# Optimization experiments

Measured on AMD Instinct MI355X. Metric: run time of the kernel, lower is better.

## Reference

```python
import jax, jax.numpy as jnp
import numpy as np

QMAX = 7.0  # 4-bit symmetric: levels in [-8, 7]

def quant4(w):
    # per-tensor symmetric 4-bit fake-quant with straight-through estimator
    s = jnp.max(jnp.abs(w)) / QMAX
    q = jnp.clip(jnp.round(w / s), -8.0, 7.0) * s
    return w + jax.lax.stop_gradient(q - w)

def setup_inputs() -> dict:
    key = jax.random.key(0)
    ks = jax.random.split(key, 7)
    B = 2048
    x = jax.random.normal(ks[0], (B, 1, 31, 16, 31), dtype=jnp.float32)
    # conv: out_ch=1, in_ch=1, kernel (5,3,5)
    w_conv = jax.random.normal(ks[1], (1, 1, 5, 3, 5), dtype=jnp.float32) * 0.1
    b_conv = jax.random.normal(ks[2], (1,), dtype=jnp.float32) * 0.1
    w_fc1 = jax.random.normal(ks[3], (128, 343), dtype=jnp.float32) * 0.05
    b_fc1 = jax.random.normal(ks[4], (128,), dtype=jnp.float32) * 0.05
    w_fc2 = jax.random.normal(ks[5], (4, 128), dtype=jnp.float32) * 0.05
    b_fc2 = jax.random.normal(ks[6], (4,), dtype=jnp.float32) * 0.05
    return {"x": x, "w_conv": w_conv, "b_conv": b_conv,
            "w_fc1": w_fc1, "b_fc1": b_fc1, "w_fc2": w_fc2, "b_fc2": b_fc2}

def reference(x, w_conv, b_conv, w_fc1, b_fc1, w_fc2, b_fc2):
    # QuantConv3d: 4-bit quantized weights, stride (2,1,2), no padding
    c1 = jax.lax.conv_general_dilated(
        x, quant4(w_conv), window_strides=(2, 1, 2), padding='VALID',
        dimension_numbers=('NCDHW', 'OIDHW', 'NCDHW'))
    c1 = c1 + b_conv.reshape(1, -1, 1, 1, 1)          # [B,1,14,14,14]
    # MaxPool3d(2)
    p1 = jax.lax.reduce_window(c1, -jnp.inf, jax.lax.max,
                               (1, 1, 2, 2, 2), (1, 1, 2, 2, 2), 'VALID')  # [B,1,7,7,7]
    f = p1.reshape(p1.shape[0], -1)                   # [B,343]
    a1 = jax.nn.relu(f @ quant4(w_fc1).T + b_fc1)     # [B,128]
    s2 = a1 @ quant4(w_fc2).T + b_fc2                 # [B,4]
    return jax.nn.softmax(s2, axis=1)
```

## Files before the change

kernel.cpp:

```cpp
#include <hip/hip_runtime.h>
#include <hip/hip_bf16.h>

#define WS_WCONV   128
#define WS_W1T     256
#define WS_W2      44160

__device__ __forceinline__ float q4(float w, float s) {
  if (s <= 0.f) return 0.f;
  float r = rintf(w / s);
  r = fminf(fmaxf(r, -8.f), 7.f);
  return r * s;
}

__global__ __launch_bounds__(256) void quant_all(
    const float* __restrict__ wconv, const float* __restrict__ w1,
    const float* __restrict__ w2, float* __restrict__ ws) {
  __shared__ float red[256];
  int b = blockIdx.x, t = threadIdx.x;
  if (b < 88) {
    const float4* w4 = (const float4*)w1;
    float m = 0.f;
    for (int i = t; i < 10976; i += 256) {
      float4 v = w4[i];
      m = fmaxf(m, fmaxf(fmaxf(fabsf(v.x), fabsf(v.y)),
                         fmaxf(fabsf(v.z), fabsf(v.w))));
    }
    red[t] = m;
    __syncthreads();
    for (int s = 128; s > 0; s >>= 1) {
      if (t < s) red[t] = fmaxf(red[t], red[t + s]);
      __syncthreads();
    }
    float s = red[0] * (1.0f / 7.0f);
    #pragma unroll
    for (int k = 0; k < 2; ++k) {
      int idx = b * 512 + k * 256 + t;
      if (idx < 43904) {
        float q = q4(w1[idx], s);
        int o = idx / 343;
        int j = idx - o * 343;
        ws[WS_W1T + j * 128 + o] = q;
      }
    }
  } else {
    float mc = (t < 75) ? fabsf(wconv[t]) : 0.f;
    float m2 = 0.f;
    for (int i = t; i < 512; i += 256) m2 = fmaxf(m2, fabsf(w2[i]));
    red[t] = mc;
    __syncthreads();
    for (int s = 128; s > 0; s >>= 1) {
      if (t < s) red[t] = fmaxf(red[t], red[t + s]);
      __syncthreads();
    }
    float sc = red[0] * (1.0f / 7.0f);
    __syncthreads();
    red[t] = m2;
    __syncthreads();
    for (int s = 128; s > 0; s >>= 1) {
      if (t < s) red[t] = fmaxf(red[t], red[t + s]);
      __syncthreads();
    }
    float s2 = red[0] * (1.0f / 7.0f);
    if (t < 75) ws[WS_WCONV + t] = q4(wconv[t], sc);
    #pragma unroll
    for (int k = 0; k < 2; ++k) {
      int idx = k * 256 + t;
      ws[WS_W2 + idx] = q4(w2[idx], s2);
    }
  }
}

__device__ __forceinline__ void conv_phase(
    const float* __restrict__ xs, const float* __restrict__ wq,
    int t, int npf, int pd_off, float bc, float* __restrict__ feat) {
  if (t >= npf) return;
  int pdl = t / 49;
  int rr  = t - pdl * 49;
  int ph  = rr / 7;
  int pw  = rr - ph * 7;
  float c[2][2][2];
  #pragma unroll
  for (int i = 0; i < 8; ++i) ((float*)c)[i] = 0.f;
  int base0 = pdl * 1984 + ph * 62 + pw * 4;
  #pragma unroll
  for (int dd = 0; dd < 7; ++dd) {
    int rbase = base0 + dd * 496;
    #pragma unroll
    for (int hh = 0; hh < 4; ++hh) {
      float row[7];
      #pragma unroll
      for (int wi = 0; wi < 7; ++wi) row[wi] = xs[rbase + hh * 31 + wi];
      #pragma unroll
      for (int odp = 0; odp < 2; ++odp) {
        int kd = dd - 2 * odp;
        if (kd < 0 || kd > 4) continue;
        #pragma unroll
        for (int ohp = 0; ohp < 2; ++ohp) {
          int kh = hh - ohp;
          if (kh < 0 || kh > 2) continue;
          #pragma unroll
          for (int owp = 0; owp < 2; ++owp) {
            float a = c[odp][ohp][owp];
            #pragma unroll
            for (int kw = 0; kw < 5; ++kw)
              a = fmaf(row[2 * owp + kw], wq[kd * 15 + kh * 5 + kw], a);
            c[odp][ohp][owp] = a;
          }
        }
      }
    }
  }
  float m = ((float*)c)[0];
  #pragma unroll
  for (int i = 1; i < 8; ++i) m = fmaxf(m, ((float*)c)[i]);
  feat[(pdl + pd_off) * 49 + rr] = m + bc;
}

__global__ __launch_bounds__(256, 4) void fused_net(
    const float* __restrict__ x, const float* __restrict__ bconv,
    const float* __restrict__ ws, const float* __restrict__ bfc1,
    const float* __restrict__ bfc2, float* __restrict__ out) {
  __shared__ float xs[9424];
  __shared__ float feat[344];
  __shared__ float fc1p[128];
  __shared__ float a1[128];
  __shared__ float s2[4];
  int t = threadIdx.x;
  int b = blockIdx.x;
  const float* wq = ws + WS_WCONV;
  float bc = bconv[0];

  {
    const float4* src = (const float4*)(x + (size_t)b * 15376);
    float4* dst = (float4*)xs;
    for (int i = t; i < 2356; i += 256) dst[i] = src[i];
    if (t == 0) feat[343] = 0.f;
  }
  __syncthreads();
  conv_phase(xs, wq, t, 196, 0, bc, feat);
  __syncthreads();
  {
    const float4* src = (const float4*)(x + (size_t)b * 15376 + 16 * 496);
    float4* dst = (float4*)xs;
    for (int i = t; i < 1860; i += 256) dst[i] = src[i];
  }
  __syncthreads();
  conv_phase(xs, wq, t, 147, 4, bc, feat);
  __syncthreads();

  int g = t >> 7, o = t & 127;
  {
    const float* w1T = ws + WS_W1T;
    int j0 = g ? 172 : 0;
    const float4* f4 = (const float4*)&feat[j0];
    const float* wp = w1T + j0 * 128 + o;
    float p0 = 0.f, p1 = 0.f, p2 = 0.f, p3 = 0.f;
    for (int q = 0; q < 43; ++q) {
      float4 ff = f4[q];
      p0 = fmaf(ff.x, wp[0],   p0);
      p1 = fmaf(ff.y, wp[128], p1);
      p2 = fmaf(ff.z, wp[256], p2);
      p3 = fmaf(ff.w, wp[384], p3);
      wp += 512;
    }
    float acc = (p0 + p1) + (p2 + p3);
    if (g) fc1p[o] = acc;
    __syncthreads();
    if (!g) a1[o] = fmaxf(acc + fc1p[o] + bfc1[o], 0.f);
  }
  __syncthreads();

  if (t < 64) {
    int cls = t & 3, kk = t >> 2;
    const float* w2 = ws + WS_W2 + cls * 128 + kk * 8;
    const float* av = a1 + kk * 8;
    float p = 0.f;
    #pragma unroll
    for (int i = 0; i < 8; ++i) p = fmaf(av[i], w2[i], p);
    p += __shfl_down(p, 32);
    p += __shfl_down(p, 16);
    p += __shfl_down(p, 8);
    p += __shfl_down(p, 4);
    if (t < 4) s2[t] = p + bfc2[t];
  }
  __syncthreads();
  if (t < 4) {
    float v0 = s2[0], v1 = s2[1], v2 = s2[2], v3 = s2[3];
    float m = fmaxf(fmaxf(v0, v1), fmaxf(v2, v3));
    float e0 = expf(v0 - m), e1 = expf(v1 - m);
    float e2 = expf(v2 - m), e3 = expf(v3 - m);
    float inv = 1.f / (e0 + e1 + e2 + e3);
    float mine = (t == 0) ? e0 : (t == 1) ? e1 : (t == 2) ? e2 : e3;
    out[b * 4 + t] = mine * inv;
  }
}

extern "C" void kernel_launch(void* const* d_in, const int* in_sizes, int n_in,
                              void* d_out, int out_size, void* d_ws, size_t ws_size,
                              hipStream_t stream) {
  const float* x     = (const float*)d_in[0];
  const float* wconv = (const float*)d_in[1];
  const float* bconv = (const float*)d_in[2];
  const float* wfc1  = (const float*)d_in[3];
  const float* bfc1  = (const float*)d_in[4];
  const float* wfc2  = (const float*)d_in[5];
  const float* bfc2  = (const float*)d_in[6];
  float* out = (float*)d_out;
  float* ws  = (float*)d_ws;

  quant_all<<<89, 256, 0, stream>>>(wconv, wfc1, wfc2, ws);
  fused_net<<<2048, 256, 0, stream>>>(x, bconv, ws, bfc1, bfc2, out);
}
```

Baseline: 227.6 us.

## Swizzle shared input rows to padded layout and prefetch second half during conv

Stores the input tile in shared memory as rows padded to 32 floats with an XOR swizzle on 4-float groups, so each conv thread reads its 7-wide window with two float4 loads instead of seven scalar loads, with fewer bank conflicts. The second half of the input is loaded into registers before the first conv phase, so the global load overlaps with compute. Small scratch arrays now alias the input buffer. The price is more address arithmetic in the scatter, higher register pressure from the prefetch registers, and a larger shared allocation that may lower occupancy.

```diff
diff --git a/kernel.cpp b/kernel.cpp
--- a/kernel.cpp
+++ b/kernel.cpp
@@ -1,5 +1,4 @@
 #include <hip/hip_runtime.h>
-#include <hip/hip_bf16.h>
 
 #define WS_WCONV   128
 #define WS_W1T     256
@@ -70,6 +69,23 @@
   }
 }
 
+__device__ __forceinline__ void scat1(float* xs, int r, int c, float v) {
+  xs[(r << 5) + (((c >> 2) ^ (r & 7)) << 2) + (c & 3)] = v;
+}
+
+__device__ __forceinline__ void scatter4(float* xs, float4 v, int i) {
+  int e0 = i << 2;
+  int r  = (int)(((unsigned)e0 * 67651u) >> 21);
+  int c  = e0 - r * 31;
+  int c1 = c + 1, r1 = r; if (c1 >= 31) { c1 -= 31; ++r1; }
+  int c2 = c + 2, r2 = r; if (c2 >= 31) { c2 -= 31; ++r2; }
+  int c3 = c + 3, r3 = r; if (c3 >= 31) { c3 -= 31; ++r3; }
+  scat1(xs, r,  c,  v.x);
+  scat1(xs, r1, c1, v.y);
+  scat1(xs, r2, c2, v.z);
+  scat1(xs, r3, c3, v.w);
+}
+
 __device__ __forceinline__ void conv_phase(
     const float* __restrict__ xs, const float* __restrict__ wq,
     int t, int npf, int pd_off, float bc, float* __restrict__ feat) {
@@ -81,15 +97,19 @@
   float c[2][2][2];
   #pragma unroll
   for (int i = 0; i < 8; ++i) ((float*)c)[i] = 0.f;
-  int base0 = pdl * 1984 + ph * 62 + pw * 4;
+  int h0 = 2 * ph;
+  int dbase = pdl * 2048;
   #pragma unroll
   for (int dd = 0; dd < 7; ++dd) {
-    int rbase = base0 + dd * 496;
+    int rb = dbase + dd * 512;
     #pragma unroll
     for (int hh = 0; hh < 4; ++hh) {
-      float row[7];
-      #pragma unroll
-      for (int wi = 0; wi < 7; ++wi) row[wi] = xs[rbase + hh * 31 + wi];
+      int h = h0 + hh;
+      int rowb = rb + (h << 5);
+      int sw = h & 7;
+      float4 A = *(const float4*)(xs + rowb + ((pw ^ sw) << 2));
+      float4 B = *(const float4*)(xs + rowb + (((pw + 1) ^ sw) << 2));
+      float row[7] = {A.x, A.y, A.z, A.w, B.x, B.y, B.z};
       #pragma unroll
       for (int odp = 0; odp < 2; ++odp) {
         int kd = dd - 2 * odp;
@@ -120,11 +140,11 @@
     const float* __restrict__ x, const float* __restrict__ bconv,
     const float* __restrict__ ws, const float* __restrict__ bfc1,
     const float* __restrict__ bfc2, float* __restrict__ out) {
-  __shared__ float xs[9424];
-  __shared__ float feat[344];
-  __shared__ float fc1p[128];
-  __shared__ float a1[128];
-  __shared__ float s2[4];
+  __shared__ alignas(16) float xs[9728];
+  __shared__ alignas(16) float feat[344];
+  float* fc1p = xs;
+  float* a1   = xs + 128;
+  float* s2   = xs + 256;
   int t = threadIdx.x;
   int b = blockIdx.x;
   const float* wq = ws + WS_WCONV;
@@ -132,19 +152,55 @@
 
   {
     const float4* src = (const float4*)(x + (size_t)b * 15376);
-    float4* dst = (float4*)xs;
-    for (int i = t; i < 2356; i += 256) dst[i] = src[i];
+    float4 v0 = src[t];
+    float4 v1 = src[t + 256];
+    float4 v2 = src[t + 512];
+    float4 v3 = src[t + 768];
+    float4 v4 = src[t + 1024];
+    float4 v5 = src[t + 1280];
+    float4 v6 = src[t + 1536];
+    float4 v7 = src[t + 1792];
+    float4 v8 = src[t + 2048];
+    bool has9 = (t + 2304) < 2356;
+    float4 v9 = has9 ? src[t + 2304] : make_float4(0.f, 0.f, 0.f, 0.f);
+    scatter4(xs, v0, t);
+    scatter4(xs, v1, t + 256);
+    scatter4(xs, v2, t + 512);
+    scatter4(xs, v3, t + 768);
+    scatter4(xs, v4, t + 1024);
+    scatter4(xs, v5, t + 1280);
+    scatter4(xs, v6, t + 1536);
+    scatter4(xs, v7, t + 1792);
+    scatter4(xs, v8, t + 2048);
+    if (has9) scatter4(xs, v9, t + 2304);
     if (t == 0) feat[343] = 0.f;
   }
   __syncthreads();
+
+  const float4* src2 = (const float4*)(x + (size_t)b * 15376 + 7936);
+  float4 p0 = src2[t];
+  float4 p1 = src2[t + 256];
+  float4 p2 = src2[t + 512];
+  float4 p3 = src2[t + 768];
+  float4 p4 = src2[t + 1024];
+  float4 p5 = src2[t + 1280];
+  float4 p6 = src2[t + 1536];
+  bool has7 = (t + 1792) < 1860;
+  float4 p7 = has7 ? src2[t + 1792] : make_float4(0.f, 0.f, 0.f, 0.f);
+
   conv_phase(xs, wq, t, 196, 0, bc, feat);
   __syncthreads();
-  {
-    const float4* src = (const float4*)(x + (size_t)b * 15376 + 16 * 496);
-    float4* dst = (float4*)xs;
-    for (int i = t; i < 1860; i += 256) dst[i] = src[i];
-  }
-  __syncthreads();
+
+  scatter4(xs, p0, t);
+  scatter4(xs, p1, t + 256);
+  scatter4(xs, p2, t + 512);
+  scatter4(xs, p3, t + 768);
+  scatter4(xs, p4, t + 1024);
+  scatter4(xs, p5, t + 1280);
+  scatter4(xs, p6, t + 1536);
+  if (has7) scatter4(xs, p7, t + 1792);
+  __syncthreads();
+
   conv_phase(xs, wq, t, 147, 4, bc, feat);
   __syncthreads();
 
@@ -154,16 +210,16 @@
     int j0 = g ? 172 : 0;
     const float4* f4 = (const float4*)&feat[j0];
     const float* wp = w1T + j0 * 128 + o;
-    float p0 = 0.f, p1 = 0.f, p2 = 0.f, p3 = 0.f;
+    float q0 = 0.f, q1 = 0.f, q2 = 0.f, q3 = 0.f;
     for (int q = 0; q < 43; ++q) {
       float4 ff = f4[q];
-      p0 = fmaf(ff.x, wp[0],   p0);
-      p1 = fmaf(ff.y, wp[128], p1);
-      p2 = fmaf(ff.z, wp[256], p2);
-      p3 = fmaf(ff.w, wp[384], p3);
+      q0 = fmaf(ff.x, wp[0],   q0);
+      q1 = fmaf(ff.y, wp[128], q1);
+      q2 = fmaf(ff.z, wp[256], q2);
+      q3 = fmaf(ff.w, wp[384], q3);
       wp += 512;
     }
-    float acc = (p0 + p1) + (p2 + p3);
+    float acc = (q0 + q1) + (q2 + q3);
     if (g) fc1p[o] = acc;
     __syncthreads();
     if (!g) a1[o] = fmaxf(acc + fc1p[o] + bfc1[o], 0.f);
@@ -172,11 +228,11 @@
 
   if (t < 64) {
     int cls = t & 3, kk = t >> 2;
-    const float* w2 = ws + WS_W2 + cls * 128 + kk * 8;
+    const float* w2p = ws + WS_W2 + cls * 128 + kk * 8;
     const float* av = a1 + kk * 8;
     float p = 0.f;
     #pragma unroll
-    for (int i = 0; i < 8; ++i) p = fmaf(av[i], w2[i], p);
+    for (int i = 0; i < 8; ++i) p = fmaf(av[i], w2p[i], p);
     p += __shfl_down(p, 32);
     p += __shfl_down(p, 16);
     p += __shfl_down(p, 8);
```

New measurement: 219.4 us. -3.6%, faster.

## Split conv input into four slabs with register prefetch to overlap loads

Applied to the files above, without the earlier changes.

The input volume is now staged into a smaller shared buffer in four depth slabs instead of two. Each next slab is prefetched from global memory into registers while the current slab is convolved. The smaller LDS footprint (about 23KB vs 40KB) together with reusing xs for the fc scratch arrays lets the launch bounds ask for 6 blocks per CU instead of 4. This aims to hide global-load latency and raise occupancy, at the cost of more register pressure from the prefetch buffers and extra barriers.

```diff
diff --git a/kernel.cpp b/kernel.cpp
--- a/kernel.cpp
+++ b/kernel.cpp
@@ -1,5 +1,4 @@
 #include <hip/hip_runtime.h>
-#include <hip/hip_bf16.h>
 
 #define WS_WCONV   128
 #define WS_W1T     256
@@ -116,36 +115,81 @@
   feat[(pdl + pd_off) * 49 + rr] = m + bc;
 }
 
-__global__ __launch_bounds__(256, 4) void fused_net(
+__global__ __launch_bounds__(256, 6) void fused_net(
     const float* __restrict__ x, const float* __restrict__ bconv,
     const float* __restrict__ ws, const float* __restrict__ bfc1,
     const float* __restrict__ bfc2, float* __restrict__ out) {
-  __shared__ float xs[9424];
-  __shared__ float feat[344];
-  __shared__ float fc1p[128];
-  __shared__ float a1[128];
-  __shared__ float s2[4];
+  __shared__ alignas(16) float xs[5456];
+  __shared__ alignas(16) float feat[344];
+  float* fc1p = xs;
+  float* a1   = xs + 128;
+  float* s2   = xs + 256;
   int t = threadIdx.x;
   int b = blockIdx.x;
   const float* wq = ws + WS_WCONV;
   float bc = bconv[0];
-
-  {
-    const float4* src = (const float4*)(x + (size_t)b * 15376);
-    float4* dst = (float4*)xs;
-    for (int i = t; i < 2356; i += 256) dst[i] = src[i];
+  const float* xb = x + (size_t)b * 15376;
+
+  const float4* s1 = (const float4*)(xb + 8 * 496);
+  float4 c1v[6];
+  #pragma unroll
+  for (int k = 0; k < 5; ++k) c1v[k] = s1[t + k * 256];
+  c1v[5] = (t < 84) ? s1[t + 1280] : make_float4(0.f, 0.f, 0.f, 0.f);
+
+  {
+    const float4* src = (const float4*)xb;
+    float4* dst = (float4*)xs;
+    #pragma unroll
+    for (int k = 0; k < 5; ++k) dst[t + k * 256] = src[t + k * 256];
+    if (t < 84) dst[t + 1280] = src[t + 1280];
     if (t == 0) feat[343] = 0.f;
   }
   __syncthreads();
-  conv_phase(xs, wq, t, 196, 0, bc, feat);
-  __syncthreads();
-  {
-    const float4* src = (const float4*)(x + (size_t)b * 15376 + 16 * 496);
-    float4* dst = (float4*)xs;
-    for (int i = t; i < 1860; i += 256) dst[i] = src[i];
-  }
-  __syncthreads();
-  conv_phase(xs, wq, t, 147, 4, bc, feat);
+
+  conv_phase(xs, wq, t, 98, 0, bc, feat);
+  __syncthreads();
+
+  {
+    float4* dst = (float4*)xs;
+    #pragma unroll
+    for (int k = 0; k < 5; ++k) dst[t + k * 256] = c1v[k];
+    if (t < 84) dst[t + 1280] = c1v[5];
+  }
+  const float4* s2p = (const float4*)(xb + 16 * 496);
+  float4 c2v[6];
+  #pragma unroll
+  for (int k = 0; k < 5; ++k) c2v[k] = s2p[t + k * 256];
+  c2v[5] = (t < 84) ? s2p[t + 1280] : make_float4(0.f, 0.f, 0.f, 0.f);
+  __syncthreads();
+
+  conv_phase(xs, wq, t, 98, 2, bc, feat);
+  __syncthreads();
+
+  {
+    float4* dst = (float4*)xs;
+    #pragma unroll
+    for (int k = 0; k < 5; ++k) dst[t + k * 256] = c2v[k];
+    if (t < 84) dst[t + 1280] = c2v[5];
+  }
+  const float4* s3p = (const float4*)(xb + 24 * 496);
+  float4 c3v[4];
+  #pragma unroll
+  for (int k = 0; k < 3; ++k) c3v[k] = s3p[t + k * 256];
+  c3v[3] = (t < 100) ? s3p[t + 768] : make_float4(0.f, 0.f, 0.f, 0.f);
+  __syncthreads();
+
+  conv_phase(xs, wq, t, 98, 4, bc, feat);
+  __syncthreads();
+
+  {
+    float4* dst = (float4*)xs;
+    #pragma unroll
+    for (int k = 0; k < 3; ++k) dst[t + k * 256] = c3v[k];
+    if (t < 100) dst[t + 768] = c3v[3];
+  }
+  __syncthreads();
+
+  conv_phase(xs, wq, t, 49, 6, bc, feat);
   __syncthreads();
 
   int g = t >> 7, o = t & 127;
@@ -154,16 +198,16 @@
     int j0 = g ? 172 : 0;
     const float4* f4 = (const float4*)&feat[j0];
     const float* wp = w1T + j0 * 128 + o;
-    float p0 = 0.f, p1 = 0.f, p2 = 0.f, p3 = 0.f;
+    float q0 = 0.f, q1 = 0.f, q2 = 0.f, q3 = 0.f;
     for (int q = 0; q < 43; ++q) {
       float4 ff = f4[q];
-      p0 = fmaf(ff.x, wp[0],   p0);
-      p1 = fmaf(ff.y, wp[128], p1);
-      p2 = fmaf(ff.z, wp[256], p2);
-      p3 = fmaf(ff.w, wp[384], p3);
+      q0 = fmaf(ff.x, wp[0],   q0);
+      q1 = fmaf(ff.y, wp[128], q1);
+      q2 = fmaf(ff.z, wp[256], q2);
+      q3 = fmaf(ff.w, wp[384], q3);
       wp += 512;
     }
-    float acc = (p0 + p1) + (p2 + p3);
+    float acc = (q0 + q1) + (q2 + q3);
     if (g) fc1p[o] = acc;
     __syncthreads();
     if (!g) a1[o] = fmaxf(acc + fc1p[o] + bfc1[o], 0.f);
@@ -172,11 +216,11 @@
 
   if (t < 64) {
     int cls = t & 3, kk = t >> 2;
-    const float* w2 = ws + WS_W2 + cls * 128 + kk * 8;
+    const float* w2p = ws + WS_W2 + cls * 128 + kk * 8;
     const float* av = a1 + kk * 8;
     float p = 0.f;
     #pragma unroll
-    for (int i = 0; i < 8; ++i) p = fmaf(av[i], w2[i], p);
+    for (int i = 0; i < 8; ++i) p = fmaf(av[i], w2p[i], p);
     p += __shfl_down(p, 32);
     p += __shfl_down(p, 16);
     p += __shfl_down(p, 8);
```

After: 258.7 us. +13.7%, slower.

## Stage full input sample in LDS and compute all conv outputs in one pass

Applied to the files above, without the earlier changes.

Each block now loads the whole 15376-float sample into shared memory at once and uses 384 threads so all 343 pooled outputs are computed in a single conv phase. This removes the second load phase and two barriers. Scratch buffers for the FC stages reuse the input tile in LDS. The cost is about 61KB of LDS per block, which cuts blocks per CU, and the occupancy hint of 4 blocks is dropped. Load latency can then no longer be overlapped with compute across blocks.

```diff
diff --git a/kernel.cpp b/kernel.cpp
--- a/kernel.cpp
+++ b/kernel.cpp
@@ -1,5 +1,4 @@
 #include <hip/hip_runtime.h>
-#include <hip/hip_bf16.h>
 
 #define WS_WCONV   128
 #define WS_W1T     256
@@ -70,10 +69,10 @@
   }
 }
 
-__device__ __forceinline__ void conv_phase(
+__device__ __forceinline__ void conv_all(
     const float* __restrict__ xs, const float* __restrict__ wq,
-    int t, int npf, int pd_off, float bc, float* __restrict__ feat) {
-  if (t >= npf) return;
+    int t, float bc, float* __restrict__ feat) {
+  if (t >= 343) return;
   int pdl = t / 49;
   int rr  = t - pdl * 49;
   int ph  = rr / 7;
@@ -113,18 +112,18 @@
   float m = ((float*)c)[0];
   #pragma unroll
   for (int i = 1; i < 8; ++i) m = fmaxf(m, ((float*)c)[i]);
-  feat[(pdl + pd_off) * 49 + rr] = m + bc;
-}
-
-__global__ __launch_bounds__(256, 4) void fused_net(
+  feat[pdl * 49 + rr] = m + bc;
+}
+
+__global__ __launch_bounds__(384) void fused_net(
     const float* __restrict__ x, const float* __restrict__ bconv,
     const float* __restrict__ ws, const float* __restrict__ bfc1,
     const float* __restrict__ bfc2, float* __restrict__ out) {
-  __shared__ float xs[9424];
-  __shared__ float feat[344];
-  __shared__ float fc1p[128];
-  __shared__ float a1[128];
-  __shared__ float s2[4];
+  __shared__ alignas(16) float xs[15376];
+  __shared__ alignas(16) float feat[344];
+  float* fc1p = xs;
+  float* a1   = xs + 128;
+  float* s2   = xs + 256;
   int t = threadIdx.x;
   int b = blockIdx.x;
   const float* wq = ws + WS_WCONV;
@@ -133,50 +132,44 @@
   {
     const float4* src = (const float4*)(x + (size_t)b * 15376);
     float4* dst = (float4*)xs;
-    for (int i = t; i < 2356; i += 256) dst[i] = src[i];
+    for (int i = t; i < 3844; i += 384) dst[i] = src[i];
     if (t == 0) feat[343] = 0.f;
   }
   __syncthreads();
-  conv_phase(xs, wq, t, 196, 0, bc, feat);
-  __syncthreads();
-  {
-    const float4* src = (const float4*)(x + (size_t)b * 15376 + 16 * 496);
-    float4* dst = (float4*)xs;
-    for (int i = t; i < 1860; i += 256) dst[i] = src[i];
-  }
-  __syncthreads();
-  conv_phase(xs, wq, t, 147, 4, bc, feat);
-  __syncthreads();
-
-  int g = t >> 7, o = t & 127;
-  {
+
+  conv_all(xs, wq, t, bc, feat);
+  __syncthreads();
+
+  int g = (t >> 7) & 1, o = t & 127;
+  float acc = 0.f;
+  if (t < 256) {
     const float* w1T = ws + WS_W1T;
     int j0 = g ? 172 : 0;
     const float4* f4 = (const float4*)&feat[j0];
     const float* wp = w1T + j0 * 128 + o;
-    float p0 = 0.f, p1 = 0.f, p2 = 0.f, p3 = 0.f;
+    float q0 = 0.f, q1 = 0.f, q2 = 0.f, q3 = 0.f;
     for (int q = 0; q < 43; ++q) {
       float4 ff = f4[q];
-      p0 = fmaf(ff.x, wp[0],   p0);
-      p1 = fmaf(ff.y, wp[128], p1);
-      p2 = fmaf(ff.z, wp[256], p2);
-      p3 = fmaf(ff.w, wp[384], p3);
+      q0 = fmaf(ff.x, wp[0],   q0);
+      q1 = fmaf(ff.y, wp[128], q1);
+      q2 = fmaf(ff.z, wp[256], q2);
+      q3 = fmaf(ff.w, wp[384], q3);
       wp += 512;
     }
-    float acc = (p0 + p1) + (p2 + p3);
+    acc = (q0 + q1) + (q2 + q3);
     if (g) fc1p[o] = acc;
-    __syncthreads();
-    if (!g) a1[o] = fmaxf(acc + fc1p[o] + bfc1[o], 0.f);
-  }
+  }
+  __syncthreads();
+  if (t < 256 && !g) a1[o] = fmaxf(acc + fc1p[o] + bfc1[o], 0.f);
   __syncthreads();
 
   if (t < 64) {
     int cls = t & 3, kk = t >> 2;
-    const float* w2 = ws + WS_W2 + cls * 128 + kk * 8;
+    const float* w2p = ws + WS_W2 + cls * 128 + kk * 8;
     const float* av = a1 + kk * 8;
     float p = 0.f;
     #pragma unroll
-    for (int i = 0; i < 8; ++i) p = fmaf(av[i], w2[i], p);
+    for (int i = 0; i < 8; ++i) p = fmaf(av[i], w2p[i], p);
     p += __shfl_down(p, 32);
     p += __shfl_down(p, 16);
     p += __shfl_down(p, 8);
@@ -209,5 +202,5 @@
   float* ws  = (float*)d_ws;
 
   quant_all<<<89, 256, 0, stream>>>(wconv, wfc1, wfc2, ws);
-  fused_net<<<2048, 256, 0, stream>>>(x, bconv, ws, bfc1, bfc2, out);
-}
+  fused_net<<<2048, 384, 0, stream>>>(x, bconv, ws, bfc1, bfc2, out);
+}
```

After: 263.1 us. +15.6%, slower.
